# Kernel tuning notes

Hardware: AMD Instinct MI355X
Metric: run time of the kernel (lower is better)

Reference implementation:

```python
import jax, jax.numpy as jnp
import numpy as np

B, T, HIN = 4, 2048, 1024
H, E = 16, 64


def setup_inputs() -> dict:
    key = jax.random.key(0)
    k1, k2, k3, k4, k5 = jax.random.split(key, 5)
    s = 1.0 / np.sqrt(HIN)
    return {
        "query": jax.random.normal(k1, (B, T, HIN), dtype=jnp.float32),
        "key_value": jax.random.normal(k2, (B, T, HIN), dtype=jnp.float32),
        "Wq": jax.random.uniform(k3, (HIN, H * E), dtype=jnp.float32, minval=-s, maxval=s),
        "Wk": jax.random.uniform(k4, (HIN, H * E), dtype=jnp.float32, minval=-s, maxval=s),
        "Wv": jax.random.uniform(k5, (HIN, H * E), dtype=jnp.float32, minval=-s, maxval=s),
    }


def reference(query, key_value, Wq, Wk, Wv):
    b, t, _ = query.shape
    scale = E ** (-0.25)  # applied to both q and k, matching e**(1/4) division
    q = (query @ Wq).reshape(b, t, H, E) * scale      # [b,t,h,e]
    k = (key_value @ Wk).reshape(b, t, H, E) * scale  # [b,t,h,e]
    v = (key_value @ Wv).reshape(b, t, H, E)          # [b,t,h,e]
    dot = jnp.einsum("bqhe,bkhe->bhqk", q, k)         # [b,h,t,t]
    attn = jax.nn.softmax(dot, axis=-1)
    out = jnp.einsum("bhqk,bkhe->bqhe", attn, v)      # [b,t,h,e]
    return out.reshape(b, t, H * E)
```

## Files before the change

### kernel.cpp

```cpp
#include <hip/hip_runtime.h>
#include <hip/hip_bf16.h>
#include <stdint.h>


typedef __bf16 bf16;
typedef __attribute__((ext_vector_type(8))) __bf16 bf16x8;
typedef __attribute__((ext_vector_type(4))) __bf16 bf16x4;
typedef __attribute__((ext_vector_type(4))) float f32x4;
typedef __attribute__((ext_vector_type(4))) short s16x4;

#define B_    4
#define T_    2048
#define HIN_  1024
#define H_    16
#define E_    64
#define NOUT_ 1024
#define LOG2E 1.4426950408889634f
#define QKSCALE 0.35355339059327373f
#define QSCALE  (QKSCALE * LOG2E)

__device__ __forceinline__ void gl_lds16(const void* g, void* l) {
  __builtin_amdgcn_global_load_lds((__attribute__((address_space(1))) void*)g,
                                   (__attribute__((address_space(3))) void*)l,
                                   16, 0, 0);
}

__global__ __launch_bounds__(256) void cvt_kernel(const float* __restrict__ Xq,
                                                  const float* __restrict__ Xkv,
                                                  bf16* __restrict__ Xb) {
  const float* src = blockIdx.y ? Xkv : Xq;
  bf16* dst = Xb + (size_t)blockIdx.y * (8192 * 1024);
  size_t i = ((size_t)blockIdx.x * 256 + threadIdx.x) * 8;
  float4 f0 = ((const float4*)(src + i))[0];
  float4 f1 = ((const float4*)(src + i))[1];
  bf16x8 t = {(bf16)f0.x, (bf16)f0.y, (bf16)f0.z, (bf16)f0.w,
              (bf16)f1.x, (bf16)f1.y, (bf16)f1.z, (bf16)f1.w};
  *(bf16x8*)(dst + i) = t;
}

__global__ __launch_bounds__(256) void wt_kernel(const float* __restrict__ Wq,
                                                 const float* __restrict__ Wk,
                                                 const float* __restrict__ Wv,
                                                 bf16* __restrict__ Wt) {
  __shared__ float s[32][33];
  const int z = blockIdx.z;
  const float* W = (z == 0) ? Wq : ((z == 1) ? Wk : Wv);
  bf16* out = Wt + (size_t)z * HIN_ * NOUT_;
  const int n0 = blockIdx.x * 32, k0 = blockIdx.y * 32;
  const int tx = threadIdx.x, ty = threadIdx.y;
#pragma unroll
  for (int i = 0; i < 4; i++)
    s[ty + i * 8][tx] = W[(size_t)(k0 + ty + i * 8) * NOUT_ + n0 + tx];
  __syncthreads();
#pragma unroll
  for (int i = 0; i < 4; i++)
    out[(size_t)(n0 + ty + i * 8) * HIN_ + k0 + tx] = (bf16)s[tx][ty + i * 8];
}

__global__ __launch_bounds__(256, 4) void proj_kernel(const bf16* __restrict__ Xb,
                                                      const bf16* __restrict__ Wt,
                                                      bf16* __restrict__ Qb,
                                                      bf16* __restrict__ Kb,
                                                      bf16* __restrict__ Vtb) {
  __shared__ bf16 As[128 * 64];
  __shared__ bf16 Bs[128 * 64];
  const int z = blockIdx.z;
  const bf16* Abase = (z == 0) ? Xb : ((z == 1) ? Xb + (size_t)8192 * 1024 : Wt + (size_t)2 * HIN_ * NOUT_);
  const bf16* Bbase = (z == 0) ? Wt : ((z == 1) ? Wt + (size_t)HIN_ * NOUT_ : Xb + (size_t)8192 * 1024);
  const int mt = (z == 2) ? blockIdx.y : blockIdx.x;
  const int nt = (z == 2) ? blockIdx.x : blockIdx.y;
  const int m0 = mt * 128, n0 = nt * 128;
  const int tid = threadIdx.x;
  const int w = tid >> 6, lane = tid & 63, quad = lane >> 4, lo = lane & 15;
  const int wm = (w >> 1) * 64, wn = (w & 1) * 64;
  const int srow = w * 8 + (lane >> 3);
  const int schunk = (lane & 7) ^ (srow & 7);

  f32x4 acc[4][4] = {};

  for (int k0 = 0; k0 < HIN_; k0 += 64) {
    __syncthreads();
#pragma unroll
    for (int j = 0; j < 4; j++) {
      int row = j * 32 + srow;
      gl_lds16(Abase + (size_t)(m0 + row) * HIN_ + k0 + schunk * 8, As + (j * 32 + w * 8) * 64);
      gl_lds16(Bbase + (size_t)(n0 + row) * HIN_ + k0 + schunk * 8, Bs + (j * 32 + w * 8) * 64);
    }
    __syncthreads();
#pragma unroll
    for (int kk = 0; kk < 2; kk++) {
      bf16x8 bfrag[4], afrag[4];
#pragma unroll
      for (int j = 0; j < 4; j++) {
        int off = ((((kk << 2) + quad) ^ (lo & 7)) << 3);
        bfrag[j] = *(const bf16x8*)(Bs + (wn + j * 16 + lo) * 64 + off);
        afrag[j] = *(const bf16x8*)(As + (wm + j * 16 + lo) * 64 + off);
      }
#pragma unroll
      for (int i = 0; i < 4; i++)
#pragma unroll
        for (int j = 0; j < 4; j++)
          acc[i][j] = __builtin_amdgcn_mfma_f32_16x16x32_bf16(afrag[i], bfrag[j], acc[i][j], 0, 0, 0);
    }
  }

#pragma unroll
  for (int i = 0; i < 4; i++)
#pragma unroll
    for (int j = 0; j < 4; j++)
#pragma unroll
      for (int r = 0; r < 4; r++) {
        int m = m0 + wm + i * 16 + quad * 4 + r;
        int n = n0 + wn + j * 16 + lo;
        float v = acc[i][j][r];
        if (z == 2) {
          int h = m >> 6, e = m & 63, b = n >> 11, t = n & 2047;
          Vtb[(((size_t)b * H_ + h) * E_ + e) * T_ + t] = (bf16)v;
        } else {
          int b = m >> 11, t = m & 2047, h = n >> 6, e = n & 63;
          if (z == 0)
            Qb[(((size_t)b * H_ + h) * T_ + t) * E_ + e] = (bf16)(v * QSCALE);
          else
            Kb[(((size_t)b * H_ + h) * T_ + t) * E_ + e] = (bf16)(v * QKSCALE);
        }
      }
}

__global__ __launch_bounds__(64, 2) void attn_kernel(const bf16* __restrict__ Qb,
                                                     const bf16* __restrict__ Kb,
                                                     const bf16* __restrict__ Vtb,
                                                     float* __restrict__ out) {
  __shared__ bf16 Ks[64 * 64];
  __shared__ bf16 Vts[64 * 64];
  const int lane = threadIdx.x & 63;
  const int quad = lane >> 4, lo = lane & 15;
  const int bh = blockIdx.x, q0 = blockIdx.y * 64;
  const bf16* Qg = Qb + (size_t)bh * T_ * E_;
  const bf16* Kg = Kb + (size_t)bh * T_ * E_;
  const bf16* Vg = Vtb + (size_t)bh * E_ * T_;
  const int srow = lane >> 3;
  const int schunk = (lane & 7) ^ (srow & 7);

  bf16x8 qf[4][2];
#pragma unroll
  for (int qi = 0; qi < 4; qi++)
#pragma unroll
    for (int ks = 0; ks < 2; ks++)
      qf[qi][ks] = *(const bf16x8*)(Qg + (size_t)(q0 + qi * 16 + lo) * E_ + ks * 32 + quad * 8);

  f32x4 acc[4][4] = {};
  float lsum[4] = {0.f, 0.f, 0.f, 0.f};

  for (int kt = 0; kt < T_ / 64; kt++) {
#pragma unroll
    for (int i = 0; i < 8; i++) {
      int row = i * 8 + srow;
      gl_lds16(Kg + (size_t)(kt * 64 + row) * E_ + schunk * 8, Ks + (i * 8) * 64);
      gl_lds16(Vg + (size_t)row * T_ + kt * 64 + schunk * 8, Vts + (i * 8) * 64);
    }
    asm volatile("s_waitcnt vmcnt(0)" ::: "memory");
    __builtin_amdgcn_sched_barrier(0);

    bf16x8 kf[4][2];
#pragma unroll
    for (int ti = 0; ti < 4; ti++)
#pragma unroll
      for (int ks = 0; ks < 2; ks++)
        kf[ti][ks] = *(const bf16x8*)(Ks + (ti * 16 + lo) * 64 + ((((ks << 2) + quad) ^ (lo & 7)) << 3));

    bf16x4 pf[4][4];
#pragma unroll
    for (int qi = 0; qi < 4; qi++) {
      f32x4 st[4] = {};
#pragma unroll
      for (int ks = 0; ks < 2; ks++)
#pragma unroll
        for (int ti = 0; ti < 4; ti++)
          st[ti] = __builtin_amdgcn_mfma_f32_16x16x32_bf16(kf[ti][ks], qf[qi][ks], st[ti], 0, 0, 0);
      float ls = 0.f;
#pragma unroll
      for (int ti = 0; ti < 4; ti++) {
        bf16x4 p4;
#pragma unroll
        for (int r = 0; r < 4; r++) {
          float p = __builtin_amdgcn_exp2f(st[ti][r]);
          ls += p;
          p4[r] = (bf16)p;
        }
        pf[qi][ti] = p4;
      }
      lsum[qi] += ls;
    }

#pragma unroll
    for (int tc = 0; tc < 4; tc++)
#pragma unroll
      for (int ej = 0; ej < 4; ej++) {
        bf16x4 vf = *(const bf16x4*)(Vts + (ej * 16 + lo) * 64 +
                                     (((tc * 2 + (quad >> 1)) ^ (lo & 7)) << 3) + (quad & 1) * 4);
#pragma unroll
        for (int qi = 0; qi < 4; qi++)
          acc[qi][ej] = __builtin_amdgcn_mfma_f32_16x16x16bf16_1k(
              __builtin_bit_cast(s16x4, pf[qi][tc]), __builtin_bit_cast(s16x4, vf),
              acc[qi][ej], 0, 0, 0);
      }
  }

  const int b = bh >> 4, h = bh & 15;
#pragma unroll
  for (int qi = 0; qi < 4; qi++) {
    float l = lsum[qi];
    l += __shfl_xor(l, 16);
    l += __shfl_xor(l, 32);
#pragma unroll
    for (int r = 0; r < 4; r++) {
      float linv = __builtin_amdgcn_rcpf(__shfl(l, quad * 4 + r));
      size_t t = q0 + qi * 16 + quad * 4 + r;
#pragma unroll
      for (int ej = 0; ej < 4; ej++)
        out[((size_t)b * T_ + t) * NOUT_ + h * E_ + ej * 16 + lo] = acc[qi][ej][r] * linv;
    }
  }
}

extern "C" void kernel_launch(void* const* d_in, const int* in_sizes, int n_in,
                              void* d_out, int out_size, void* d_ws, size_t ws_size,
                              hipStream_t stream) {
  const float* Xq  = (const float*)d_in[0];
  const float* Xkv = (const float*)d_in[1];
  const float* Wq  = (const float*)d_in[2];
  const float* Wk  = (const float*)d_in[3];
  const float* Wv  = (const float*)d_in[4];
  float* out = (float*)d_out;

  char* ws = (char*)d_ws;
  bf16* Qb  = (bf16*)(ws);
  bf16* Kb  = (bf16*)(ws + ((size_t)16 << 20));
  bf16* Vtb = (bf16*)(ws + ((size_t)32 << 20));
  bf16* Wt  = (bf16*)(ws + ((size_t)48 << 20));
  bf16* Xb  = (bf16*)d_out;

  hipLaunchKernelGGL(cvt_kernel, dim3(4096, 2), dim3(256), 0, stream, Xq, Xkv, Xb);
  hipLaunchKernelGGL(wt_kernel, dim3(32, 32, 3), dim3(32, 8), 0, stream, Wq, Wk, Wv, Wt);
  hipLaunchKernelGGL(proj_kernel, dim3(64, 8, 3), dim3(256), 0, stream, Xb, Wt, Qb, Kb, Vtb);
  hipLaunchKernelGGL(attn_kernel, dim3(64, 32), dim3(64), 0, stream, Qb, Kb, Vtb, out);
}
```

Baseline: 265.2 us.

## Switch attention kernel to 32x32x16 MFMA tiles with permlane32 P relayout

Rewrites both attention matmuls to use 32x32x16 bf16 MFMA instead of 16x16x32 and 16x16x16, cutting the instruction count and the LDS fragment loads per tile. Softmax probabilities are packed with v_cvt_pk_bf16_f32 and rearranged with permlane32_swap so the S accumulator layout matches the A operand of the PV MFMA without going through LDS. The row-sum reduction and output indexing are adapted to the 32x32 accumulator layout. This raises per-lane register pressure, since the accumulators are now 16-wide.

```diff
diff --git a/kernel.cpp b/kernel.cpp
--- a/kernel.cpp
+++ b/kernel.cpp
@@ -5,9 +5,10 @@
 
 typedef __bf16 bf16;
 typedef __attribute__((ext_vector_type(8))) __bf16 bf16x8;
-typedef __attribute__((ext_vector_type(4))) __bf16 bf16x4;
 typedef __attribute__((ext_vector_type(4))) float f32x4;
-typedef __attribute__((ext_vector_type(4))) short s16x4;
+typedef __attribute__((ext_vector_type(16))) float f32x16;
+typedef __attribute__((ext_vector_type(4))) unsigned int u32x4;
+typedef __attribute__((ext_vector_type(2))) unsigned int u32x2;
 
 #define B_    4
 #define T_    2048
@@ -133,7 +134,7 @@
   __shared__ bf16 Ks[64 * 64];
   __shared__ bf16 Vts[64 * 64];
   const int lane = threadIdx.x & 63;
-  const int quad = lane >> 4, lo = lane & 15;
+  const int l31 = lane & 31, hi = lane >> 5;
   const int bh = blockIdx.x, q0 = blockIdx.y * 64;
   const bf16* Qg = Qb + (size_t)bh * T_ * E_;
   const bf16* Kg = Kb + (size_t)bh * T_ * E_;
@@ -141,15 +142,15 @@
   const int srow = lane >> 3;
   const int schunk = (lane & 7) ^ (srow & 7);
 
-  bf16x8 qf[4][2];
-#pragma unroll
-  for (int qi = 0; qi < 4; qi++)
-#pragma unroll
-    for (int ks = 0; ks < 2; ks++)
-      qf[qi][ks] = *(const bf16x8*)(Qg + (size_t)(q0 + qi * 16 + lo) * E_ + ks * 32 + quad * 8);
-
-  f32x4 acc[4][4] = {};
-  float lsum[4] = {0.f, 0.f, 0.f, 0.f};
+  bf16x8 qf[2][4];
+#pragma unroll
+  for (int qb = 0; qb < 2; qb++)
+#pragma unroll
+    for (int ks = 0; ks < 4; ks++)
+      qf[qb][ks] = *(const bf16x8*)(Qg + (size_t)(q0 + qb * 32 + l31) * E_ + ks * 16 + hi * 8);
+
+  f32x16 acc[2][2] = {};
+  float lsum[2] = {0.f, 0.f};
 
   for (int kt = 0; kt < T_ / 64; kt++) {
 #pragma unroll
@@ -161,66 +162,76 @@
     asm volatile("s_waitcnt vmcnt(0)" ::: "memory");
     __builtin_amdgcn_sched_barrier(0);
 
-    bf16x8 kf[4][2];
-#pragma unroll
-    for (int ti = 0; ti < 4; ti++)
-#pragma unroll
-      for (int ks = 0; ks < 2; ks++)
-        kf[ti][ks] = *(const bf16x8*)(Ks + (ti * 16 + lo) * 64 + ((((ks << 2) + quad) ^ (lo & 7)) << 3));
-
-    bf16x4 pf[4][4];
-#pragma unroll
-    for (int qi = 0; qi < 4; qi++) {
-      f32x4 st[4] = {};
-#pragma unroll
-      for (int ks = 0; ks < 2; ks++)
-#pragma unroll
-        for (int ti = 0; ti < 4; ti++)
-          st[ti] = __builtin_amdgcn_mfma_f32_16x16x32_bf16(kf[ti][ks], qf[qi][ks], st[ti], 0, 0, 0);
-      float ls = 0.f;
-#pragma unroll
-      for (int ti = 0; ti < 4; ti++) {
-        bf16x4 p4;
-#pragma unroll
-        for (int r = 0; r < 4; r++) {
-          float p = __builtin_amdgcn_exp2f(st[ti][r]);
-          ls += p;
-          p4[r] = (bf16)p;
+    bf16x8 kf[2][4];
+#pragma unroll
+    for (int tb = 0; tb < 2; tb++)
+#pragma unroll
+      for (int ks = 0; ks < 4; ks++)
+        kf[tb][ks] = *(const bf16x8*)(Ks + (tb * 32 + l31) * 64 +
+                                      (((2 * ks + hi) ^ (l31 & 7)) << 3));
+
+    bf16x8 pf[2][4];
+#pragma unroll
+    for (int qb = 0; qb < 2; qb++) {
+#pragma unroll
+      for (int tb = 0; tb < 2; tb++) {
+        f32x16 st = {};
+#pragma unroll
+        for (int ks = 0; ks < 4; ks++)
+          st = __builtin_amdgcn_mfma_f32_32x32x16_bf16(kf[tb][ks], qf[qb][ks], st, 0, 0, 0);
+        float ex[16];
+        float ls = 0.f;
+#pragma unroll
+        for (int r = 0; r < 16; r++) {
+          ex[r] = __builtin_amdgcn_exp2f(st[r]);
+          ls += ex[r];
         }
-        pf[qi][ti] = p4;
-      }
-      lsum[qi] += ls;
+        lsum[qb] += ls;
+        unsigned int u[4][2];
+#pragma unroll
+        for (int g = 0; g < 4; g++)
+#pragma unroll
+          for (int p = 0; p < 2; p++)
+            asm("v_cvt_pk_bf16_f32 %0, %1, %2"
+                : "=v"(u[g][p]) : "v"(ex[4 * g + 2 * p]), "v"(ex[4 * g + 2 * p + 1]));
+#pragma unroll
+        for (int c2 = 0; c2 < 2; c2++) {
+          u32x2 s0 = __builtin_amdgcn_permlane32_swap(u[2 * c2][0], u[2 * c2 + 1][0], false, false);
+          u32x2 s1 = __builtin_amdgcn_permlane32_swap(u[2 * c2][1], u[2 * c2 + 1][1], false, false);
+          u32x4 wv = {s0[0], s1[0], s0[1], s1[1]};
+          pf[qb][tb * 2 + c2] = __builtin_bit_cast(bf16x8, wv);
+        }
+      }
     }
 
 #pragma unroll
     for (int tc = 0; tc < 4; tc++)
 #pragma unroll
-      for (int ej = 0; ej < 4; ej++) {
-        bf16x4 vf = *(const bf16x4*)(Vts + (ej * 16 + lo) * 64 +
-                                     (((tc * 2 + (quad >> 1)) ^ (lo & 7)) << 3) + (quad & 1) * 4);
-#pragma unroll
-        for (int qi = 0; qi < 4; qi++)
-          acc[qi][ej] = __builtin_amdgcn_mfma_f32_16x16x16bf16_1k(
-              __builtin_bit_cast(s16x4, pf[qi][tc]), __builtin_bit_cast(s16x4, vf),
-              acc[qi][ej], 0, 0, 0);
+      for (int eb = 0; eb < 2; eb++) {
+        bf16x8 vf = *(const bf16x8*)(Vts + (eb * 32 + l31) * 64 +
+                                     (((2 * tc + hi) ^ (l31 & 7)) << 3));
+#pragma unroll
+        for (int qb = 0; qb < 2; qb++)
+          acc[qb][eb] = __builtin_amdgcn_mfma_f32_32x32x16_bf16(pf[qb][tc], vf, acc[qb][eb], 0, 0, 0);
       }
   }
 
+#pragma unroll
+  for (int qb = 0; qb < 2; qb++)
+    lsum[qb] += __shfl_xor(lsum[qb], 32);
+
   const int b = bh >> 4, h = bh & 15;
 #pragma unroll
-  for (int qi = 0; qi < 4; qi++) {
-    float l = lsum[qi];
-    l += __shfl_xor(l, 16);
-    l += __shfl_xor(l, 32);
-#pragma unroll
-    for (int r = 0; r < 4; r++) {
-      float linv = __builtin_amdgcn_rcpf(__shfl(l, quad * 4 + r));
-      size_t t = q0 + qi * 16 + quad * 4 + r;
-#pragma unroll
-      for (int ej = 0; ej < 4; ej++)
-        out[((size_t)b * T_ + t) * NOUT_ + h * E_ + ej * 16 + lo] = acc[qi][ej][r] * linv;
-    }
-  }
+  for (int qb = 0; qb < 2; qb++)
+#pragma unroll
+    for (int r = 0; r < 16; r++) {
+      int qrow = (r & 3) + 8 * (r >> 2) + 4 * hi;
+      float linv = __builtin_amdgcn_rcpf(__shfl(lsum[qb], qrow));
+      size_t t = q0 + qb * 32 + qrow;
+#pragma unroll
+      for (int eb = 0; eb < 2; eb++)
+        out[((size_t)b * T_ + t) * NOUT_ + h * E_ + eb * 32 + l31] = acc[qb][eb][r] * linv;
+    }
 }
 
 extern "C" void kernel_launch(void* const* d_in, const int* in_sizes, int n_in,
```

Result: faster. 248.7 us (median of 2 runs) (-6.2%).
